# Optimization experiments

Hardware: AMD Instinct MI355X
Metric: run time of the kernel (lower is better)

Reference implementation:

```python
import jax, jax.numpy as jnp
import numpy as np
import math

B, S, NUM_HEADS, HEAD_SIZE = 4, 2048, 16, 64
EMB = NUM_HEADS * HEAD_SIZE  # 1024


def setup_inputs() -> dict:
    key = jax.random.key(0)
    k0, k1, k2, k3 = jax.random.split(key, 4)
    scale = 1.0 / math.sqrt(EMB)
    return {
        "hidden_states": jax.random.normal(k0, (B, S, EMB), dtype=jnp.float32),
        "qkv_w": jax.random.normal(k1, (EMB, 3 * EMB), dtype=jnp.float32) * scale,
        "qkv_b": jnp.zeros((3 * EMB,), dtype=jnp.float32),
        "wo_w": jax.random.normal(k2, (EMB, EMB), dtype=jnp.float32) * scale,
        "wo_b": jnp.zeros((EMB,), dtype=jnp.float32),
        "mask": jax.random.randint(k3, (B, S), 0, 2, dtype=jnp.int64)
        if jax.config.jax_enable_x64 else jax.random.randint(k3, (B, S), 0, 2, dtype=jnp.int32),
    }


def reference(hidden_states, qkv_w, qkv_b, wo_w, wo_b, mask):
    b, s, e = hidden_states.shape
    h, d = NUM_HEADS, HEAD_SIZE
    qkv = hidden_states @ qkv_w + qkv_b            # [b, s, 3e]
    q, k, v = jnp.split(qkv, 3, axis=-1)
    # split heads: [b, s, e] -> [b, h, s, d]
    split = lambda t: t.reshape(b, s, h, d).transpose(0, 2, 1, 3)
    q, k, v = split(q), split(k), split(v)
    # naive attention: full [b, h, s, s] score matrix, scaled by sqrt(head_size)
    scores = jnp.einsum("bhqd,bhkd->bhqk", q, k) / jnp.sqrt(jnp.asarray(d, q.dtype))
    # torch code repeats the [b, s] padding mask into [b, h, s, s]; it masks KEYS:
    # position j with mask[b, j] == 0 is -inf for all queries and heads.
    scores = jnp.where(mask[:, None, None, :] == 0, -jnp.inf, scores)
    attn = jax.nn.softmax(scores, axis=-1)
    out = jnp.einsum("bhqk,bhkd->bhqd", attn, v)   # [b, h, s, d]
    out = out.transpose(0, 2, 1, 3).reshape(b, s, e)  # merge heads
    return out @ wo_w + wo_b
```

## Files before the change

### kernel.cpp

```cpp
#include <hip/hip_runtime.h>
#include <math.h>

typedef __bf16 bf16;
typedef __bf16 bf16x4 __attribute__((ext_vector_type(4)));
typedef __bf16 bf16x8 __attribute__((ext_vector_type(8)));
typedef float floatx4 __attribute__((ext_vector_type(4)));

#define MFMA_BF16(a, b, c) __builtin_amdgcn_mfma_f32_16x16x32_bf16((a), (b), (c), 0, 0, 0)

__device__ inline void gload16(const void* g, void* l) {
  __builtin_amdgcn_global_load_lds(
      (const __attribute__((address_space(1))) void*)g,
      (__attribute__((address_space(3))) void*)l, 16, 0, 0);
}

__device__ inline int detect_i64(const void* m_) {
  const unsigned int* m = (const unsigned int*)m_;
  unsigned int o = 0;
  for (int i = 1; i < 256; i += 2) o |= m[i];
  return o == 0;
}

__device__ inline int xcd_swizzle(int bid, int nwg) {
  return (bid & 7) * (nwg >> 3) + (bid >> 3);
}

__global__ void wsplit(const float* __restrict__ in, bf16* __restrict__ outh,
                       bf16* __restrict__ outl, int R, int C) {
  __shared__ float tile[32][33];
  int bx = blockIdx.x * 32, by = blockIdx.y * 32;
  int tx = threadIdx.x, ty = threadIdx.y;
#pragma unroll
  for (int i = 0; i < 32; i += 8)
    tile[ty + i][tx] = in[(size_t)(by + ty + i) * C + bx + tx];
  __syncthreads();
#pragma unroll
  for (int i = 0; i < 32; i += 8) {
    float x = tile[tx][ty + i];
    bf16 h = (bf16)x;
    size_t oi = (size_t)(bx + ty + i) * R + by + tx;
    outh[oi] = h;
    outl[oi] = (bf16)(x - (float)h);
  }
}

template <int MODE>
__global__ __launch_bounds__(256) void gemm(
    const void* __restrict__ Av, const bf16* __restrict__ Bhg,
    const bf16* __restrict__ Blg, const float* __restrict__ bias,
    void* __restrict__ Cq, bf16* __restrict__ Ck, bf16* __restrict__ Cv,
    int M, int N, int K) {
  constexpr int APAD = (MODE == 1) ? 40 : 32;
  __shared__ __align__(16) bf16 Ah[2][128][APAD];
  __shared__ __align__(16) bf16 Bh[2][128][32];
  __shared__ __align__(16) bf16 Bl[2][128][32];

  int tid = threadIdx.x;
  int wave = tid >> 6, lane = tid & 63;
  int quad = lane >> 4, c = lane & 15;
  int wrow = (wave >> 1) * 64, wcol = (wave & 1) * 64;

  int nwg = gridDim.x * gridDim.y;
  int bid = blockIdx.x + gridDim.x * blockIdx.y;
  int nb = xcd_swizzle(bid, nwg);
  int m0 = (nb / gridDim.x) * 128, n0 = (nb % gridDim.x) * 128;

  int srow = lane >> 2;
  int ql8 = (((lane & 3) ^ ((lane >> 3) & 3)) * 8);
  int rswz = (c >> 1) & 3;

  floatx4 zero4 = {0.f, 0.f, 0.f, 0.f};
  floatx4 acc[4][4];
#pragma unroll
  for (int i = 0; i < 4; ++i)
#pragma unroll
    for (int j = 0; j < 4; ++j) acc[i][j] = zero4;

  floatx4 aR[4];

#define STAGE_B(buf, kk)                                                    \
  {                                                                         \
    _Pragma("unroll") for (int u = 0; u < 2; ++u) {                         \
      int ch = wave * 2 + u;                                                \
      size_t gi = (size_t)(n0 + ch * 16 + srow) * K + (kk) + ql8;           \
      gload16(&Bhg[gi], &Bh[buf][ch * 16][0]);                              \
      gload16(&Blg[gi], &Bl[buf][ch * 16][0]);                              \
    }                                                                       \
  }
#define STAGE_A_DMA(buf, kk)                                                \
  {                                                                         \
    _Pragma("unroll") for (int u = 0; u < 2; ++u) {                         \
      int ch = wave * 2 + u;                                                \
      size_t gi = (size_t)(m0 + ch * 16 + srow) * K + (kk) + ql8;           \
      gload16((const bf16*)Av + gi, &Ah[buf][ch * 16][0]);                  \
    }                                                                       \
  }
#define ISSUE_A(kk)                                                         \
  {                                                                         \
    const float* Af = (const float*)Av;                                     \
    _Pragma("unroll") for (int p = 0; p < 2; ++p) {                         \
      int off = p * 2048 + tid * 8;                                         \
      int r = off >> 5, cc = off & 31;                                      \
      size_t gi = (size_t)(m0 + r) * K + (kk) + cc;                         \
      aR[p * 2] = *(const floatx4*)&Af[gi];                                 \
      aR[p * 2 + 1] = *(const floatx4*)&Af[gi + 4];                         \
    }                                                                       \
  }
#define WRITE_A(buf)                                                        \
  {                                                                         \
    _Pragma("unroll") for (int p = 0; p < 2; ++p) {                         \
      int off = p * 2048 + tid * 8;                                         \
      int r = off >> 5, cc = off & 31;                                      \
      bf16x8 h;                                                             \
      _Pragma("unroll") for (int uu = 0; uu < 4; ++uu) {                    \
        h[uu] = (bf16)aR[p * 2][uu];                                        \
        h[4 + uu] = (bf16)aR[p * 2 + 1][uu];                                \
      }                                                                     \
      *(bf16x8*)&Ah[buf][r][cc] = h;                                        \
    }                                                                       \
  }

  STAGE_B(0, 0);
  if constexpr (MODE == 1) {
    ISSUE_A(0);
    WRITE_A(0);
  } else {
    STAGE_A_DMA(0, 0);
  }
  __syncthreads();

  int nk = K / 32;
  int cur = 0;
  for (int t = 0; t < nk; ++t) {
    int kn = (t + 1) * 32;
    bool has_next = (t + 1 < nk);
    if (has_next) {
      STAGE_B(cur ^ 1, kn);
      if constexpr (MODE == 1) {
        ISSUE_A(kn);
      } else {
        STAGE_A_DMA(cur ^ 1, kn);
      }
    }

    bf16x8 ah[4], bh[4], bl[4];
#pragma unroll
    for (int i = 0; i < 4; ++i) {
      if constexpr (MODE == 1)
        ah[i] = *(const bf16x8*)&Ah[cur][wrow + i * 16 + c][quad * 8];
      else
        ah[i] = *(const bf16x8*)&Ah[cur][wrow + i * 16 + c][(quad ^ rswz) * 8];
    }
#pragma unroll
    for (int j = 0; j < 4; ++j) {
      bh[j] = *(const bf16x8*)&Bh[cur][wcol + j * 16 + c][(quad ^ rswz) * 8];
      bl[j] = *(const bf16x8*)&Bl[cur][wcol + j * 16 + c][(quad ^ rswz) * 8];
    }
#pragma unroll
    for (int i = 0; i < 4; ++i)
#pragma unroll
      for (int j = 0; j < 4; ++j)
        acc[i][j] = MFMA_BF16(ah[i], bh[j], acc[i][j]);
#pragma unroll
    for (int i = 0; i < 4; ++i)
#pragma unroll
      for (int j = 0; j < 4; ++j)
        acc[i][j] = MFMA_BF16(ah[i], bl[j], acc[i][j]);

    if (has_next) {
      if constexpr (MODE == 1) WRITE_A(cur ^ 1);
      __syncthreads();
      cur ^= 1;
    }
  }
#undef STAGE_B
#undef STAGE_A_DMA
#undef ISSUE_A
#undef WRITE_A

#pragma unroll
  for (int i = 0; i < 4; ++i) {
#pragma unroll
    for (int j = 0; j < 4; ++j) {
      int col = n0 + wcol + j * 16 + c;
      float bvv = bias[col];
#pragma unroll
      for (int r = 0; r < 4; ++r) {
        int row = m0 + wrow + i * 16 + quad * 4 + r;
        float v = acc[i][j][r] + bvv;
        if constexpr (MODE == 0) {
          ((float*)Cq)[(size_t)row * N + col] = v;
        } else {
          int which = col >> 10;
          int h = (col >> 6) & 15;
          int d = col & 63;
          int b = row >> 11;
          int s = row & 2047;
          if (which == 0) {
            ((bf16*)Cq)[((size_t)(b * 2048 + s)) * 1024 + h * 64 + d] = (bf16)v;
          } else if (which == 1) {
            Ck[((size_t)(b * 16 + h) * 2048 + s) * 64 + d] = (bf16)v;
          } else {
            Cv[((size_t)(b * 16 + h) * 64 + d) * 2048 + s] = (bf16)v;
          }
        }
      }
    }
  }
}

__global__ __launch_bounds__(256) void attn_fused(
    bf16* QO, const bf16* __restrict__ Kg, const bf16* __restrict__ Vg,
    const void* __restrict__ mask) {
  __shared__ __align__(16) bf16 Qs[64][72];
  __shared__ __align__(16) bf16 Ks[64][72];
  __shared__ __align__(16) bf16 Vts[64][72];
  __shared__ __align__(16) bf16 Ps[64][72];
  __shared__ __align__(16) float abuf[64];

  const int i64 = detect_i64(mask);

  int tid = threadIdx.x;
  int wave = tid >> 6, lane = tid & 63;
  int quad = lane >> 4, c = lane & 15;

  int nwg = gridDim.x * gridDim.y;
  int bid = blockIdx.x + gridDim.x * blockIdx.y;
  int nb = xcd_swizzle(bid, nwg);
  int qt = nb & 31, bh = nb >> 5;

  int b = bh >> 4, h = bh & 15;
  int q0 = qt * 64;
  bf16* Qp = QO + (size_t)b * 2048 * 1024 + h * 64;
  const bf16* Kp = Kg + (size_t)bh * 2048 * 64;
  const bf16* Vp = Vg + (size_t)bh * 64 * 2048;

#pragma unroll
  for (int p = 0; p < 2; ++p) {
    int off = p * 2048 + tid * 8;
    int r = off >> 6, cc = off & 63;
    *(bf16x8*)&Qs[r][cc] = *(const bf16x8*)&Qp[(size_t)(q0 + r) * 1024 + cc];
  }

  float lacc = 0.f;
  floatx4 zero4 = {0.f, 0.f, 0.f, 0.f};
  floatx4 o[4];
#pragma unroll
  for (int jd = 0; jd < 4; ++jd) o[jd] = zero4;

  for (int kt = 0; kt < 32; ++kt) {
    int k0 = kt * 64;
    __syncthreads();
#pragma unroll
    for (int p = 0; p < 2; ++p) {
      int off = p * 2048 + tid * 8;
      int r = off >> 6, cc = off & 63;
      *(bf16x8*)&Ks[r][cc] = *(const bf16x8*)&Kp[(size_t)(k0 + r) * 64 + cc];
      *(bf16x8*)&Vts[r][cc] = *(const bf16x8*)&Vp[(size_t)r * 2048 + k0 + cc];
    }
    if (tid < 64) {
      int idx = b * 2048 + k0 + tid;
      int mv = i64 ? (int)((const long long*)mask)[idx]
                   : ((const int*)mask)[idx];
      abuf[tid] = mv ? -12.0f : -1e30f;
    }
    __syncthreads();

    floatx4 st[4];
#pragma unroll
    for (int j = 0; j < 4; ++j) st[j] = zero4;
#pragma unroll
    for (int dstep = 0; dstep < 64; dstep += 32) {
      bf16x8 bq = *(const bf16x8*)&Qs[wave * 16 + c][dstep + quad * 8];
#pragma unroll
      for (int j = 0; j < 4; ++j) {
        bf16x8 ak = *(const bf16x8*)&Ks[j * 16 + c][dstep + quad * 8];
        st[j] = MFMA_BF16(ak, bq, st[j]);
      }
    }

#pragma unroll
    for (int j = 0; j < 4; ++j) {
      floatx4 am = *(const floatx4*)&abuf[j * 16 + quad * 4];
      bf16x4 pk;
#pragma unroll
      for (int r = 0; r < 4; ++r) {
        float pv = __expf(fmaf(st[j][r], 0.125f, am[r]));
        pk[r] = (bf16)pv;
        lacc += pv;
      }
      *(bf16x4*)&Ps[wave * 16 + c][j * 16 + quad * 4] = pk;
    }

#pragma unroll
    for (int kk = 0; kk < 64; kk += 32) {
      bf16x8 ap = *(const bf16x8*)&Ps[wave * 16 + c][kk + quad * 8];
#pragma unroll
      for (int jd = 0; jd < 4; ++jd) {
        bf16x8 bv = *(const bf16x8*)&Vts[jd * 16 + c][kk + quad * 8];
        o[jd] = MFMA_BF16(ap, bv, o[jd]);
      }
    }
  }

  lacc += __shfl_xor(lacc, 16, 64);
  lacc += __shfl_xor(lacc, 32, 64);

#pragma unroll
  for (int r = 0; r < 4; ++r) {
    float lr = __shfl(lacc, quad * 4 + r, 64);
    float inv_l = 1.0f / fmaxf(lr, 1e-30f);
    int row = q0 + wave * 16 + quad * 4 + r;
#pragma unroll
    for (int jd = 0; jd < 4; ++jd) {
      float ov = o[jd][r] * inv_l;
      Qp[(size_t)row * 1024 + jd * 16 + c] = (bf16)ov;
    }
  }
}

extern "C" void kernel_launch(void* const* d_in, const int* in_sizes, int n_in,
                              void* d_out, int out_size, void* d_ws, size_t ws_size,
                              hipStream_t stream) {
  (void)in_sizes; (void)n_in; (void)out_size;
  const float* hs    = (const float*)d_in[0];
  const float* qkv_w = (const float*)d_in[1];
  const float* qkv_b = (const float*)d_in[2];
  const float* wo_w  = (const float*)d_in[3];
  const float* wo_b  = (const float*)d_in[4];
  const void*  mask  = d_in[5];

  if (ws_size < 33554432) return;

  bf16* kbuf  = (bf16*)d_ws;
  bf16* wqh   = (bf16*)((char*)d_ws + 16777216);
  bf16* wql   = wqh + (size_t)3145728;
  bf16* woh   = wql + (size_t)3145728;
  bf16* wol   = woh + (size_t)1048576;
  bf16* vbuf  = (bf16*)d_out + (size_t)8388608;
  bf16* obuf  = (bf16*)d_ws;

  wsplit<<<dim3(96, 32), dim3(32, 8), 0, stream>>>(qkv_w, wqh, wql, 1024, 3072);
  wsplit<<<dim3(32, 32), dim3(32, 8), 0, stream>>>(wo_w, woh, wol, 1024, 1024);

  gemm<1><<<dim3(24, 64), 256, 0, stream>>>(
      hs, wqh, wql, qkv_b, d_out, kbuf, vbuf, 8192, 3072, 1024);

  attn_fused<<<dim3(32, 64), 256, 0, stream>>>(
      (bf16*)d_out, kbuf, vbuf, mask);

  (void)hipMemcpyAsync(d_ws, d_out, (size_t)16777216, hipMemcpyDeviceToDevice,
                       stream);

  gemm<0><<<dim3(8, 64), 256, 0, stream>>>(
      obuf, woh, wol, wo_b, d_out, nullptr, nullptr, 8192, 1024, 1024);
}
```

Measured before the change: 419.4 us.

## Keep Q fragments in registers and software-pipeline K/V tile loads in attention

Drops the Q shared-memory tile and loads each wave's Q fragments straight into registers once. Restructures the key loop so the V tile's global load is issued before the QK^T MFMAs, and the next K tile and mask are prefetched into registers during the PV MFMAs, then written to LDS. The aim is to hide global memory latency behind compute and cut LDS usage. In exchange it adds register pressure, and the new barrier placement has to stay correct for the Ps, Vts and Ks reuse across iterations.

```diff
diff --git a/kernel.cpp b/kernel.cpp
--- a/kernel.cpp
+++ b/kernel.cpp
@@ -212,7 +212,6 @@
 __global__ __launch_bounds__(256) void attn_fused(
     bf16* QO, const bf16* __restrict__ Kg, const bf16* __restrict__ Vg,
     const void* __restrict__ mask) {
-  __shared__ __align__(16) bf16 Qs[64][72];
   __shared__ __align__(16) bf16 Ks[64][72];
   __shared__ __align__(16) bf16 Vts[64][72];
   __shared__ __align__(16) bf16 Ps[64][72];
@@ -235,47 +234,52 @@
   const bf16* Kp = Kg + (size_t)bh * 2048 * 64;
   const bf16* Vp = Vg + (size_t)bh * 64 * 2048;
 
+  bf16x8 qf[2];
+#pragma unroll
+  for (int ds = 0; ds < 2; ++ds)
+    qf[ds] = *(const bf16x8*)&Qp[(size_t)(q0 + wave * 16 + c) * 1024 +
+                                 ds * 32 + quad * 8];
+
+  float lacc = 0.f;
+  floatx4 zero4 = {0.f, 0.f, 0.f, 0.f};
+  floatx4 o[4];
+#pragma unroll
+  for (int jd = 0; jd < 4; ++jd) o[jd] = zero4;
+
 #pragma unroll
   for (int p = 0; p < 2; ++p) {
     int off = p * 2048 + tid * 8;
     int r = off >> 6, cc = off & 63;
-    *(bf16x8*)&Qs[r][cc] = *(const bf16x8*)&Qp[(size_t)(q0 + r) * 1024 + cc];
-  }
-
-  float lacc = 0.f;
-  floatx4 zero4 = {0.f, 0.f, 0.f, 0.f};
-  floatx4 o[4];
-#pragma unroll
-  for (int jd = 0; jd < 4; ++jd) o[jd] = zero4;
+    *(bf16x8*)&Ks[r][cc] = *(const bf16x8*)&Kp[(size_t)r * 64 + cc];
+  }
+  if (tid < 64) {
+    int idx = b * 2048 + tid;
+    int mv = i64 ? (int)((const long long*)mask)[idx]
+                 : ((const int*)mask)[idx];
+    abuf[tid] = mv ? -12.0f : -1e30f;
+  }
+  __syncthreads();
 
   for (int kt = 0; kt < 32; ++kt) {
     int k0 = kt * 64;
-    __syncthreads();
+
+    bf16x8 vstage[2];
 #pragma unroll
     for (int p = 0; p < 2; ++p) {
       int off = p * 2048 + tid * 8;
       int r = off >> 6, cc = off & 63;
-      *(bf16x8*)&Ks[r][cc] = *(const bf16x8*)&Kp[(size_t)(k0 + r) * 64 + cc];
-      *(bf16x8*)&Vts[r][cc] = *(const bf16x8*)&Vp[(size_t)r * 2048 + k0 + cc];
-    }
-    if (tid < 64) {
-      int idx = b * 2048 + k0 + tid;
-      int mv = i64 ? (int)((const long long*)mask)[idx]
-                   : ((const int*)mask)[idx];
-      abuf[tid] = mv ? -12.0f : -1e30f;
-    }
-    __syncthreads();
+      vstage[p] = *(const bf16x8*)&Vp[(size_t)r * 2048 + k0 + cc];
+    }
 
     floatx4 st[4];
 #pragma unroll
     for (int j = 0; j < 4; ++j) st[j] = zero4;
 #pragma unroll
-    for (int dstep = 0; dstep < 64; dstep += 32) {
-      bf16x8 bq = *(const bf16x8*)&Qs[wave * 16 + c][dstep + quad * 8];
+    for (int ds = 0; ds < 2; ++ds) {
 #pragma unroll
       for (int j = 0; j < 4; ++j) {
-        bf16x8 ak = *(const bf16x8*)&Ks[j * 16 + c][dstep + quad * 8];
-        st[j] = MFMA_BF16(ak, bq, st[j]);
+        bf16x8 ak = *(const bf16x8*)&Ks[j * 16 + c][ds * 32 + quad * 8];
+        st[j] = MFMA_BF16(ak, qf[ds], st[j]);
       }
     }
 
@@ -293,6 +297,26 @@
     }
 
 #pragma unroll
+    for (int p = 0; p < 2; ++p) {
+      int off = p * 2048 + tid * 8;
+      int r = off >> 6, cc = off & 63;
+      *(bf16x8*)&Vts[r][cc] = vstage[p];
+    }
+    __syncthreads();
+
+    bf16x8 kstage[2];
+    bool more = (kt + 1) < 32;
+    int kn = k0 + 64;
+    if (more) {
+#pragma unroll
+      for (int p = 0; p < 2; ++p) {
+        int off = p * 2048 + tid * 8;
+        int r = off >> 6, cc = off & 63;
+        kstage[p] = *(const bf16x8*)&Kp[(size_t)(kn + r) * 64 + cc];
+      }
+    }
+
+#pragma unroll
     for (int kk = 0; kk < 64; kk += 32) {
       bf16x8 ap = *(const bf16x8*)&Ps[wave * 16 + c][kk + quad * 8];
 #pragma unroll
@@ -300,6 +324,22 @@
         bf16x8 bv = *(const bf16x8*)&Vts[jd * 16 + c][kk + quad * 8];
         o[jd] = MFMA_BF16(ap, bv, o[jd]);
       }
+    }
+
+    if (more) {
+#pragma unroll
+      for (int p = 0; p < 2; ++p) {
+        int off = p * 2048 + tid * 8;
+        int r = off >> 6, cc = off & 63;
+        *(bf16x8*)&Ks[r][cc] = kstage[p];
+      }
+      if (tid < 64) {
+        int idx = b * 2048 + kn + tid;
+        int mv = i64 ? (int)((const long long*)mask)[idx]
+                     : ((const int*)mask)[idx];
+        abuf[tid] = mv ? -12.0f : -1e30f;
+      }
+      __syncthreads();
     }
   }
 
```

Result: no change. 411.9 us (-1.8%).

## Split keys across waves in attention and keep P in registers

Applied to the files above, without the earlier changes.

The attention kernel now gives each wave a 16-key slice of every 64-key tile, across all 64 queries. K, V and Q fragments are loaded straight from global memory into registers, so the per-tile LDS staging and both __syncthreads per tile are gone. The softmax probabilities feed a transposed PV product through a 16x16x16 bf16 MFMA without a round trip through LDS. The partial outputs and row sums from the four waves are then reduced in LDS before normalising and writing. The cost is serialised cross-wave reductions at the end, more accumulator registers, and narrower MFMAs for the PV step.

```diff
diff --git a/kernel.cpp b/kernel.cpp
--- a/kernel.cpp
+++ b/kernel.cpp
@@ -5,8 +5,25 @@
 typedef __bf16 bf16x4 __attribute__((ext_vector_type(4)));
 typedef __bf16 bf16x8 __attribute__((ext_vector_type(8)));
 typedef float floatx4 __attribute__((ext_vector_type(4)));
+typedef short shortx4 __attribute__((ext_vector_type(4)));
 
 #define MFMA_BF16(a, b, c) __builtin_amdgcn_mfma_f32_16x16x32_bf16((a), (b), (c), 0, 0, 0)
+
+__device__ inline floatx4 MFMA_PV(bf16x4 a, bf16x4 b, floatx4 c) {
+#if __has_builtin(__builtin_amdgcn_mfma_f32_16x16x16_bf16)
+  return __builtin_amdgcn_mfma_f32_16x16x16_bf16(a, b, c, 0, 0, 0);
+#elif __has_builtin(__builtin_amdgcn_mfma_f32_16x16x16bf16_1k)
+  shortx4 as, bs;
+  __builtin_memcpy(&as, &a, 8);
+  __builtin_memcpy(&bs, &b, 8);
+  return __builtin_amdgcn_mfma_f32_16x16x16bf16_1k(as, bs, c, 0, 0, 0);
+#else
+  bf16 z = (bf16)0.f;
+  bf16x8 a8 = {a[0], a[1], a[2], a[3], z, z, z, z};
+  bf16x8 b8 = {b[0], b[1], b[2], b[3], z, z, z, z};
+  return MFMA_BF16(a8, b8, c);
+#endif
+}
 
 __device__ inline void gload16(const void* g, void* l) {
   __builtin_amdgcn_global_load_lds(
@@ -212,11 +229,10 @@
 __global__ __launch_bounds__(256) void attn_fused(
     bf16* QO, const bf16* __restrict__ Kg, const bf16* __restrict__ Vg,
     const void* __restrict__ mask) {
-  __shared__ __align__(16) bf16 Qs[64][72];
-  __shared__ __align__(16) bf16 Ks[64][72];
-  __shared__ __align__(16) bf16 Vts[64][72];
-  __shared__ __align__(16) bf16 Ps[64][72];
-  __shared__ __align__(16) float abuf[64];
+  __shared__ __align__(16) char smem[17664];
+  float* abuf_all = (float*)smem;
+  float(*Osum)[65] = (float(*)[65])smem;
+  float* l_lds = (float*)(smem + 16640);
 
   const int i64 = detect_i64(mask);
 
@@ -236,87 +252,107 @@
   const bf16* Vp = Vg + (size_t)bh * 64 * 2048;
 
 #pragma unroll
-  for (int p = 0; p < 2; ++p) {
-    int off = p * 2048 + tid * 8;
-    int r = off >> 6, cc = off & 63;
-    *(bf16x8*)&Qs[r][cc] = *(const bf16x8*)&Qp[(size_t)(q0 + r) * 1024 + cc];
-  }
-
-  float lacc = 0.f;
+  for (int i = 0; i < 8; ++i) {
+    int key = tid * 8 + i;
+    int idx = b * 2048 + key;
+    int mv = i64 ? (int)((const long long*)mask)[idx]
+                 : ((const int*)mask)[idx];
+    abuf_all[key] = mv ? -12.0f : -1e30f;
+  }
+
+  bf16x8 qf[8];
+#pragma unroll
+  for (int qt2 = 0; qt2 < 4; ++qt2)
+#pragma unroll
+    for (int ds = 0; ds < 2; ++ds)
+      qf[qt2 * 2 + ds] = *(const bf16x8*)&Qp[(size_t)(q0 + qt2 * 16 + c) * 1024 +
+                                             ds * 32 + quad * 8];
+
   floatx4 zero4 = {0.f, 0.f, 0.f, 0.f};
-  floatx4 o[4];
-#pragma unroll
-  for (int jd = 0; jd < 4; ++jd) o[jd] = zero4;
+  floatx4 acc[4][4];
+#pragma unroll
+  for (int i = 0; i < 4; ++i)
+#pragma unroll
+    for (int j = 0; j < 4; ++j) acc[i][j] = zero4;
+  float lacc[4] = {0.f, 0.f, 0.f, 0.f};
+
+  __syncthreads();
 
   for (int kt = 0; kt < 32; ++kt) {
-    int k0 = kt * 64;
+    int ks = kt * 64 + wave * 16;
+
+    const bf16* kp = &Kp[(size_t)(ks + c) * 64 + quad * 8];
+    bf16x8 ak0 = *(const bf16x8*)kp;
+    bf16x8 ak1 = *(const bf16x8*)(kp + 32);
+
+    bf16x4 av[4];
+#pragma unroll
+    for (int dt = 0; dt < 4; ++dt)
+      av[dt] = *(const bf16x4*)&Vp[(size_t)(dt * 16 + c) * 2048 + ks + quad * 4];
+
+    floatx4 am = *(const floatx4*)&abuf_all[ks + quad * 4];
+
+#pragma unroll
+    for (int qt2 = 0; qt2 < 4; ++qt2) {
+      floatx4 st = zero4;
+      st = MFMA_BF16(ak0, qf[qt2 * 2], st);
+      st = MFMA_BF16(ak1, qf[qt2 * 2 + 1], st);
+
+      bf16x4 pk;
+#pragma unroll
+      for (int r = 0; r < 4; ++r) {
+        float pv = __expf(fmaf(st[r], 0.125f, am[r]));
+        lacc[qt2] += pv;
+        pk[r] = (bf16)pv;
+      }
+
+#pragma unroll
+      for (int dt = 0; dt < 4; ++dt)
+        acc[dt][qt2] = MFMA_PV(av[dt], pk, acc[dt][qt2]);
+    }
+  }
+
+#pragma unroll
+  for (int qt2 = 0; qt2 < 4; ++qt2) {
+    lacc[qt2] += __shfl_xor(lacc[qt2], 16, 64);
+    lacc[qt2] += __shfl_xor(lacc[qt2], 32, 64);
+  }
+  if (quad == 0) {
+#pragma unroll
+    for (int qt2 = 0; qt2 < 4; ++qt2)
+      l_lds[wave * 64 + qt2 * 16 + c] = lacc[qt2];
+  }
+  __syncthreads();
+
+  for (int w2 = 0; w2 < 4; ++w2) {
+    if (wave == w2) {
+#pragma unroll
+      for (int dt = 0; dt < 4; ++dt)
+#pragma unroll
+        for (int qt2 = 0; qt2 < 4; ++qt2)
+#pragma unroll
+          for (int r = 0; r < 4; ++r) {
+            int row = dt * 16 + quad * 4 + r, col = qt2 * 16 + c;
+            if (w2 == 0)
+              Osum[row][col] = acc[dt][qt2][r];
+            else
+              Osum[row][col] += acc[dt][qt2][r];
+          }
+    }
     __syncthreads();
-#pragma unroll
-    for (int p = 0; p < 2; ++p) {
-      int off = p * 2048 + tid * 8;
-      int r = off >> 6, cc = off & 63;
-      *(bf16x8*)&Ks[r][cc] = *(const bf16x8*)&Kp[(size_t)(k0 + r) * 64 + cc];
-      *(bf16x8*)&Vts[r][cc] = *(const bf16x8*)&Vp[(size_t)r * 2048 + k0 + cc];
-    }
-    if (tid < 64) {
-      int idx = b * 2048 + k0 + tid;
-      int mv = i64 ? (int)((const long long*)mask)[idx]
-                   : ((const int*)mask)[idx];
-      abuf[tid] = mv ? -12.0f : -1e30f;
-    }
-    __syncthreads();
-
-    floatx4 st[4];
-#pragma unroll
-    for (int j = 0; j < 4; ++j) st[j] = zero4;
-#pragma unroll
-    for (int dstep = 0; dstep < 64; dstep += 32) {
-      bf16x8 bq = *(const bf16x8*)&Qs[wave * 16 + c][dstep + quad * 8];
-#pragma unroll
-      for (int j = 0; j < 4; ++j) {
-        bf16x8 ak = *(const bf16x8*)&Ks[j * 16 + c][dstep + quad * 8];
-        st[j] = MFMA_BF16(ak, bq, st[j]);
-      }
-    }
-
-#pragma unroll
-    for (int j = 0; j < 4; ++j) {
-      floatx4 am = *(const floatx4*)&abuf[j * 16 + quad * 4];
-      bf16x4 pk;
-#pragma unroll
-      for (int r = 0; r < 4; ++r) {
-        float pv = __expf(fmaf(st[j][r], 0.125f, am[r]));
-        pk[r] = (bf16)pv;
-        lacc += pv;
-      }
-      *(bf16x4*)&Ps[wave * 16 + c][j * 16 + quad * 4] = pk;
-    }
-
-#pragma unroll
-    for (int kk = 0; kk < 64; kk += 32) {
-      bf16x8 ap = *(const bf16x8*)&Ps[wave * 16 + c][kk + quad * 8];
-#pragma unroll
-      for (int jd = 0; jd < 4; ++jd) {
-        bf16x8 bv = *(const bf16x8*)&Vts[jd * 16 + c][kk + quad * 8];
-        o[jd] = MFMA_BF16(ap, bv, o[jd]);
-      }
-    }
-  }
-
-  lacc += __shfl_xor(lacc, 16, 64);
-  lacc += __shfl_xor(lacc, 32, 64);
-
-#pragma unroll
-  for (int r = 0; r < 4; ++r) {
-    float lr = __shfl(lacc, quad * 4 + r, 64);
-    float inv_l = 1.0f / fmaxf(lr, 1e-30f);
-    int row = q0 + wave * 16 + quad * 4 + r;
-#pragma unroll
-    for (int jd = 0; jd < 4; ++jd) {
-      float ov = o[jd][r] * inv_l;
-      Qp[(size_t)row * 1024 + jd * 16 + c] = (bf16)ov;
-    }
-  }
+  }
+
+  int q = tid >> 2, dblk = tid & 3;
+  float l = l_lds[0 * 64 + q] + l_lds[1 * 64 + q] + l_lds[2 * 64 + q] +
+            l_lds[3 * 64 + q];
+  float inv = 1.0f / fmaxf(l, 1e-30f);
+  bf16x8 h0, h1;
+#pragma unroll
+  for (int i = 0; i < 8; ++i) h0[i] = (bf16)(Osum[dblk * 16 + i][q] * inv);
+#pragma unroll
+  for (int i = 0; i < 8; ++i) h1[i] = (bf16)(Osum[dblk * 16 + 8 + i][q] * inv);
+  *(bf16x8*)&Qp[(size_t)(q0 + q) * 1024 + dblk * 16] = h0;
+  *(bf16x8*)&Qp[(size_t)(q0 + q) * 1024 + dblk * 16 + 8] = h1;
 }
 
 extern "C" void kernel_launch(void* const* d_in, const int* in_sizes, int n_in,
```

Result: slower. 482.9 us (+15.1%).
